# Optimization experiments

Hardware: AMD Instinct MI355X
Metric: run time of the kernel (lower is better)

## Reference

```python
import jax, jax.numpy as jnp
import numpy as np

N_ATOM, N_TOKEN = 1024, 256
C_S, C_Z, C_ATOM, C_ATOM_PAIR = 384, 128, 128, 16
EPS = 1e-5


def _layer_norm(x, w, b):
    m = jnp.mean(x, axis=-1, keepdims=True)
    v = jnp.mean(jnp.square(x - m), axis=-1, keepdims=True)
    return (x - m) * jax.lax.rsqrt(v + EPS) * w + b


def setup_inputs() -> dict:
    key = jax.random.key(0)
    ks = jax.random.split(key, 12)
    # one-hot atom -> token map (each atom belongs to exactly one token)
    tok_idx = jnp.sort(jax.random.randint(ks[0], (N_ATOM,), 0, N_TOKEN))
    a2t = jax.nn.one_hot(tok_idx, N_TOKEN, dtype=jnp.float32)  # [n_atom, n_token]
    return {
        "atom_to_token_index": a2t,
        "cl": jax.random.normal(ks[1], (N_ATOM, C_ATOM), jnp.float32),
        "plm": jax.random.normal(ks[2], (N_ATOM, N_ATOM, C_ATOM_PAIR), jnp.float32),
        "ql": jax.random.normal(ks[3], (N_ATOM, C_ATOM), jnp.float32),
        "s_trunk": jax.random.normal(ks[4], (N_TOKEN, C_S), jnp.float32),
        "zij": jax.random.normal(ks[5], (N_TOKEN, N_TOKEN, C_Z), jnp.float32),
        "rl": jax.random.normal(ks[6], (N_ATOM, 3), jnp.float32),
        "ln_s_w": jnp.ones((C_S,), jnp.float32),
        "ln_s_b": jnp.zeros((C_S,), jnp.float32),
        "W_s": jax.random.normal(ks[7], (C_S, C_ATOM), jnp.float32) / np.sqrt(C_S),
        "ln_z_w": jnp.ones((C_Z,), jnp.float32),
        "ln_z_b": jnp.zeros((C_Z,), jnp.float32),
        "W_z": jax.random.normal(ks[8], (C_Z, C_ATOM_PAIR), jnp.float32) / np.sqrt(C_Z),
        "W_r": jax.random.normal(ks[9], (3, C_ATOM), jnp.float32) / np.sqrt(3.0),
    }


def reference(atom_to_token_index, cl, plm, ql, s_trunk, zij, rl,
              ln_s_w, ln_s_b, W_s, ln_z_w, ln_z_b, W_z, W_r):
    a2t = atom_to_token_index  # one-hot [n_atom, n_token]
    # cl += Linear_s(LN_s(sum_t s_trunk[t] * a2t[a,t]))  (token->atom broadcast)
    s_atom = jnp.einsum('tc,at->ac', s_trunk, a2t)  # [n_atom, c_s]
    cl = cl + _layer_norm(s_atom, ln_s_w, ln_s_b) @ W_s
    # plm += Linear_z(LN_z(sum_{t,m} zij[t,m] * a2t[a,t] * a2t[b,m]))
    z_at = jnp.einsum('tmc,at->amc', zij, a2t)      # [n_atom, n_token, c_z]
    z_ab = jnp.einsum('amc,bm->abc', z_at, a2t)     # [n_atom, n_atom, c_z]
    plm = plm + _layer_norm(z_ab, ln_z_w, ln_z_b) @ W_z
    # ql += Linear_r(rl)
    ql = ql + rl @ W_r
    return (cl, plm, ql)
```

## Files before the change

### kernel.cpp

```cpp
#include <hip/hip_runtime.h>
#include <hip/hip_bf16.h>

#define NA 1024
#define NT 256
#define CS 384
#define CZ 128
#define CA 128
#define CP 16

typedef __attribute__((ext_vector_type(8))) short short8;
typedef __attribute__((ext_vector_type(4))) float f32x4;

__device__ __forceinline__ float bfu(unsigned short v){ return __uint_as_float(((unsigned)v) << 16); }
__device__ __forceinline__ unsigned short f2bf(float f){
  unsigned u = __float_as_uint(f);
  return (unsigned short)((u + 0x7fffu + ((u >> 16) & 1u)) >> 16);
}
__device__ __forceinline__ unsigned pack2(float lo, float hi){
  return (unsigned)f2bf(lo) | ((unsigned)f2bf(hi) << 16);
}

__device__ __forceinline__ int lbound(const unsigned short* tokL, int key){
  int lo = 0, hi = NA;
  while (lo < hi) { int mid = (lo + hi) >> 1; if ((int)tokL[mid] < key) lo = mid + 1; else hi = mid; }
  return lo;
}

__global__ __launch_bounds__(256) void prep_kernel(
    const float* __restrict__ a2t,
    const float* __restrict__ s_trunk,
    const float* __restrict__ lnsw,
    const float* __restrict__ lnsb,
    const float* __restrict__ Ws,
    unsigned short* __restrict__ tok16,
    unsigned short* __restrict__ ytok)
{
  __shared__ float redS[4], redQ[4];
  __shared__ float lnbuf[CS];
  __shared__ float part[CA];

  const int blk  = blockIdx.x;
  const int tid  = threadIdx.x;
  const int lane = tid & 63;
  const int wv   = tid >> 6;

  if (blk < 256) {
    int a = blk * 4 + wv;
    float4 u = ((const float4*)(a2t + (size_t)a * NT))[lane];
    bool hit = (u.x != 0.f) | (u.y != 0.f) | (u.z != 0.f) | (u.w != 0.f);
    unsigned long long m = __ballot(hit);
    int fl = __ffsll(m) - 1;
    if (lane == fl) {
      int t = lane * 4;
      if (u.x != 0.f)      {  }
      else if (u.y != 0.f) t += 1;
      else if (u.z != 0.f) t += 2;
      else                 t += 3;
      tok16[a] = (unsigned short)t;
    }
  } else {
    int tk = blk - 256;
    float f0 = 0.f, f1 = 0.f;
    if (tid < 192) {
      float2 v = ((const float2*)(s_trunk + (size_t)tk * CS))[tid];
      f0 = v.x; f1 = v.y;
    }
    float s = f0 + f1;
    float q = f0 * f0 + f1 * f1;
    #pragma unroll
    for (int m = 1; m < 64; m <<= 1) { s += __shfl_xor(s, m); q += __shfl_xor(q, m); }
    if (lane == 0) { redS[wv] = s; redQ[wv] = q; }
    __syncthreads();
    if (tid == 0) {
      float S = redS[0] + redS[1] + redS[2] + redS[3];
      float Q = redQ[0] + redQ[1] + redQ[2] + redQ[3];
      float mean = S * (1.f / 384.f);
      float var  = Q * (1.f / 384.f) - mean * mean;
      redS[0] = mean;
      redQ[0] = rsqrtf(var + 1e-5f);
    }
    __syncthreads();
    float mean = redS[0], rstd = redQ[0];
    if (tid < 192) {
      float2 w2 = ((const float2*)lnsw)[tid];
      float2 b2 = ((const float2*)lnsb)[tid];
      lnbuf[2 * tid]     = fmaf((f0 - mean) * rstd, w2.x, b2.x);
      lnbuf[2 * tid + 1] = fmaf((f1 - mean) * rstd, w2.y, b2.y);
    }
    __syncthreads();
    int j = tid & 127, half = tid >> 7;
    float acc = 0.f;
    int c0 = half * 192;
    #pragma unroll 8
    for (int c = c0; c < c0 + 192; ++c)
      acc = fmaf(lnbuf[c], Ws[(size_t)c * CA + j], acc);
    if (half) part[j] = acc;
    __syncthreads();
    if (!half) ytok[(size_t)tk * CA + j] = f2bf(acc + part[j]);
  }
}

__global__ __launch_bounds__(256) void main_kernel(
    const float* __restrict__ cl,
    const float* __restrict__ plm,
    const float* __restrict__ ql,
    const float* __restrict__ rl,
    const float* __restrict__ Wr,
    const float* __restrict__ zij,
    const float* __restrict__ lnzw,
    const float* __restrict__ lnzb,
    const float* __restrict__ Wz,
    const unsigned short* __restrict__ tok16,
    const unsigned short* __restrict__ ytok,
    float* __restrict__ out)
{
  const int blk = blockIdx.x;
  const int tid = threadIdx.x;

  if (blk < 1024) {
    __shared__ unsigned short tokL[NA];
    __shared__ unsigned short stage[4 * 16 * 136];
    __shared__ float wlds[64 * 16];

    const int lane = tid & 63;
    const int wv   = tid >> 6;
    const int t    = blk >> 2;
    const int m0   = (blk & 3) << 6;

    ((uint2*)tokL)[tid] = ((const uint2*)tok16)[tid];
    __syncthreads();

    int s = lbound(tokL, t);
    int e = lbound(tokL, t + 1);
    if (s == e) return;
    int S = lbound(tokL, m0);
    int E = lbound(tokL, m0 + 64);
    if (S == E) return;

    {
      int r = lane >> 2, q = lane & 3;
      int mrow = m0 + wv * 16 + r;
      const float4* zp = (const float4*)(zij + ((size_t)t * NT + mrow) * CZ + q * 32);
      float x[32];
      float sm = 0.f, ss = 0.f;
      #pragma unroll
      for (int i = 0; i < 8; ++i) {
        float4 v = zp[i];
        x[4 * i]     = v.x; x[4 * i + 1] = v.y;
        x[4 * i + 2] = v.z; x[4 * i + 3] = v.w;
        sm += (v.x + v.y) + (v.z + v.w);
        ss = fmaf(v.x, v.x, ss); ss = fmaf(v.y, v.y, ss);
        ss = fmaf(v.z, v.z, ss); ss = fmaf(v.w, v.w, ss);
      }
      sm += __shfl_xor(sm, 1); sm += __shfl_xor(sm, 2);
      ss += __shfl_xor(ss, 1); ss += __shfl_xor(ss, 2);
      float mean = sm * (1.f / 128.f);
      float var  = ss * (1.f / 128.f) - mean * mean;
      float rstd = rsqrtf(var + 1e-5f);
      unsigned short* st = stage + wv * 2176 + r * 136 + q * 32;
      const float4* lwp = (const float4*)(lnzw + q * 32);
      const float4* lbp = (const float4*)(lnzb + q * 32);
      #pragma unroll
      for (int i = 0; i < 4; ++i) {
        float4 lw0 = lwp[2 * i], lw1 = lwp[2 * i + 1];
        float4 lb0 = lbp[2 * i], lb1 = lbp[2 * i + 1];
        int c = i * 8;
        unsigned o0 = pack2(fmaf((x[c]     - mean) * rstd, lw0.x, lb0.x),
                            fmaf((x[c + 1] - mean) * rstd, lw0.y, lb0.y));
        unsigned o1 = pack2(fmaf((x[c + 2] - mean) * rstd, lw0.z, lb0.z),
                            fmaf((x[c + 3] - mean) * rstd, lw0.w, lb0.w));
        unsigned o2 = pack2(fmaf((x[c + 4] - mean) * rstd, lw1.x, lb1.x),
                            fmaf((x[c + 5] - mean) * rstd, lw1.y, lb1.y));
        unsigned o3 = pack2(fmaf((x[c + 6] - mean) * rstd, lw1.z, lb1.z),
                            fmaf((x[c + 7] - mean) * rstd, lw1.w, lb1.w));
        uint4 ov; ov.x = o0; ov.y = o1; ov.z = o2; ov.w = o3;
        ((uint4*)st)[i] = ov;
      }
      __syncthreads();
      int h = lane >> 4, lm = lane & 15;
      short8 bfrag[4];
      #pragma unroll
      for (int kk = 0; kk < 4; ++kk)
        #pragma unroll
        for (int jj = 0; jj < 8; ++jj)
          bfrag[kk][jj] = (short)f2bf(Wz[(size_t)(kk * 32 + h * 8 + jj) * CP + lm]);
      const unsigned short* sb = stage + wv * 2176;
      f32x4 acc = {0.f, 0.f, 0.f, 0.f};
      #pragma unroll
      for (int kk = 0; kk < 4; ++kk) {
        short8 af = *(const short8*)(sb + lm * 136 + kk * 32 + h * 8);
        acc = __builtin_amdgcn_mfma_f32_16x16x32_bf16(af, bfrag[kk], acc, 0, 0, 0);
      }
      #pragma unroll
      for (int jj = 0; jj < 4; ++jj)
        wlds[(wv * 16 + h * 4 + jj) * 16 + lm] = acc[jj];
    }
    __syncthreads();

    const float4* plm4 = (const float4*)plm;
    float4* out4 = (float4*)(out + (size_t)NA * CA);
    int ntask = (E - S) * 4;
    for (int a = s; a < e; ++a) {
      size_t rowbase = ((size_t)a << 10);
      for (int task = tid; task < ntask; task += 256) {
        int b = S + (task >> 2), quar = task & 3;
        int m = ((int)tokL[b] - m0) & 63;
        const float* w = wlds + m * 16 + quar * 4;
        size_t p4 = (rowbase + b) * 4 + quar;
        float4 pv = plm4[p4];
        float4 ov;
        ov.x = pv.x + w[0]; ov.y = pv.y + w[1];
        ov.z = pv.z + w[2]; ov.w = pv.w + w[3];
        out4[p4] = ov;
      }
    }
  } else if (blk < 1536) {
    int idx = (blk - 1024) * 256 + tid;
    int a = idx >> 7, j = idx & 127;
    int ta = (int)tok16[a] & 255;
    out[idx] = cl[idx] + bfu(ytok[(size_t)ta * CA + j]);
  } else {
    int idx = (blk - 1536) * 256 + tid;
    int a = idx >> 7, j = idx & 127;
    float r0 = rl[a * 3 + 0], r1 = rl[a * 3 + 1], r2 = rl[a * 3 + 2];
    float v = ql[idx];
    v = fmaf(r0, Wr[j], v);
    v = fmaf(r1, Wr[CA + j], v);
    v = fmaf(r2, Wr[2 * CA + j], v);
    out[(size_t)NA * CA + (size_t)NA * NA * CP + idx] = v;
  }
}

extern "C" void kernel_launch(void* const* d_in, const int* in_sizes, int n_in,
                              void* d_out, int out_size, void* d_ws, size_t ws_size,
                              hipStream_t stream) {
  const float* a2t     = (const float*)d_in[0];
  const float* cl      = (const float*)d_in[1];
  const float* plm     = (const float*)d_in[2];
  const float* ql      = (const float*)d_in[3];
  const float* s_trunk = (const float*)d_in[4];
  const float* zij     = (const float*)d_in[5];
  const float* rl      = (const float*)d_in[6];
  const float* lnsw    = (const float*)d_in[7];
  const float* lnsb    = (const float*)d_in[8];
  const float* Ws      = (const float*)d_in[9];
  const float* lnzw    = (const float*)d_in[10];
  const float* lnzb    = (const float*)d_in[11];
  const float* Wz      = (const float*)d_in[12];
  const float* Wr      = (const float*)d_in[13];
  float* out = (float*)d_out;

  unsigned short* tok16 = (unsigned short*)d_ws;
  unsigned short* ytok  = (unsigned short*)d_ws + NA;

  prep_kernel<<<512, 256, 0, stream>>>(a2t, s_trunk, lnsw, lnsb, Ws, tok16, ytok);
  main_kernel<<<2048, 256, 0, stream>>>(cl, plm, ql, rl, Wr, zij, lnzw, lnzb, Wz,
                                        tok16, ytok, out);
}
```

Before: 220.7 us.

## Split atom rows across two blocks per tile and batch plm loads

Each (token, m-chunk) tile now runs as two blocks, each handling alternating atom rows, which doubles the grid of pair blocks to spread the memory-bound plm streaming across more workgroups. The staging buffer and the weight table share one LDS allocation to cut shared-memory use, which needs an extra barrier. The inner loop issues four plm loads before any stores to raise memory-level parallelism. The cost is that each block recomputes the LayerNorm and MFMA projection for its tile, doubling that work.

After: 213.5 us. 3.3% less time.

```diff
diff --git a/kernel.cpp b/kernel.cpp
--- a/kernel.cpp
+++ b/kernel.cpp
@@ -117,22 +117,24 @@
   const int blk = blockIdx.x;
   const int tid = threadIdx.x;
 
-  if (blk < 1024) {
+  if (blk < 2048) {
     __shared__ unsigned short tokL[NA];
-    __shared__ unsigned short stage[4 * 16 * 136];
-    __shared__ float wlds[64 * 16];
+    __shared__ __align__(16) unsigned short ubuf[4 * 16 * 136];
+    unsigned short* stage = ubuf;
+    float* wlds = (float*)ubuf;
 
     const int lane = tid & 63;
     const int wv   = tid >> 6;
-    const int t    = blk >> 2;
-    const int m0   = (blk & 3) << 6;
+    const int t    = blk >> 3;
+    const int m0   = ((blk >> 1) & 3) << 6;
+    const int slot = blk & 1;
 
     ((uint2*)tokL)[tid] = ((const uint2*)tok16)[tid];
     __syncthreads();
 
     int s = lbound(tokL, t);
     int e = lbound(tokL, t + 1);
-    if (s == e) return;
+    if (s + slot >= e) return;
     int S = lbound(tokL, m0);
     int E = lbound(tokL, m0 + 64);
     if (S == E) return;
@@ -185,12 +187,15 @@
         for (int jj = 0; jj < 8; ++jj)
           bfrag[kk][jj] = (short)f2bf(Wz[(size_t)(kk * 32 + h * 8 + jj) * CP + lm]);
       const unsigned short* sb = stage + wv * 2176;
+      short8 af[4];
+      #pragma unroll
+      for (int kk = 0; kk < 4; ++kk)
+        af[kk] = *(const short8*)(sb + lm * 136 + kk * 32 + h * 8);
       f32x4 acc = {0.f, 0.f, 0.f, 0.f};
       #pragma unroll
-      for (int kk = 0; kk < 4; ++kk) {
-        short8 af = *(const short8*)(sb + lm * 136 + kk * 32 + h * 8);
-        acc = __builtin_amdgcn_mfma_f32_16x16x32_bf16(af, bfrag[kk], acc, 0, 0, 0);
-      }
+      for (int kk = 0; kk < 4; ++kk)
+        acc = __builtin_amdgcn_mfma_f32_16x16x32_bf16(af[kk], bfrag[kk], acc, 0, 0, 0);
+      __syncthreads();
       #pragma unroll
       for (int jj = 0; jj < 4; ++jj)
         wlds[(wv * 16 + h * 4 + jj) * 16 + lm] = acc[jj];
@@ -199,28 +204,42 @@
 
     const float4* plm4 = (const float4*)plm;
     float4* out4 = (float4*)(out + (size_t)NA * CA);
-    int ntask = (E - S) * 4;
-    for (int a = s; a < e; ++a) {
+    const int ntask = (E - S) * 4;
+    for (int a = s + slot; a < e; a += 2) {
       size_t rowbase = ((size_t)a << 10);
-      for (int task = tid; task < ntask; task += 256) {
-        int b = S + (task >> 2), quar = task & 3;
-        int m = ((int)tokL[b] - m0) & 63;
-        const float* w = wlds + m * 16 + quar * 4;
-        size_t p4 = (rowbase + b) * 4 + quar;
-        float4 pv = plm4[p4];
-        float4 ov;
-        ov.x = pv.x + w[0]; ov.y = pv.y + w[1];
-        ov.z = pv.z + w[2]; ov.w = pv.w + w[3];
-        out4[p4] = ov;
+      for (int base = 0; base < ntask; base += 1024) {
+        float4 pv[4], wv4[4];
+        size_t idx4[4];
+        bool act[4];
+        #pragma unroll
+        for (int j = 0; j < 4; ++j) {
+          int task = base + j * 256 + tid;
+          act[j] = (task < ntask);
+          int tt = act[j] ? task : 0;
+          int b = S + (tt >> 2), quar = tt & 3;
+          int m = ((int)tokL[b] - m0) & 63;
+          idx4[j] = (rowbase + b) * 4 + quar;
+          wv4[j] = *(const float4*)(wlds + m * 16 + quar * 4);
+          pv[j]  = plm4[idx4[j]];
+        }
+        #pragma unroll
+        for (int j = 0; j < 4; ++j) {
+          if (act[j]) {
+            float4 ov;
+            ov.x = pv[j].x + wv4[j].x; ov.y = pv[j].y + wv4[j].y;
+            ov.z = pv[j].z + wv4[j].z; ov.w = pv[j].w + wv4[j].w;
+            out4[idx4[j]] = ov;
+          }
+        }
       }
     }
-  } else if (blk < 1536) {
-    int idx = (blk - 1024) * 256 + tid;
+  } else if (blk < 2560) {
+    int idx = (blk - 2048) * 256 + tid;
     int a = idx >> 7, j = idx & 127;
     int ta = (int)tok16[a] & 255;
     out[idx] = cl[idx] + bfu(ytok[(size_t)ta * CA + j]);
   } else {
-    int idx = (blk - 1536) * 256 + tid;
+    int idx = (blk - 2560) * 256 + tid;
     int a = idx >> 7, j = idx & 127;
     float r0 = rl[a * 3 + 0], r1 = rl[a * 3 + 1], r2 = rl[a * 3 + 2];
     float v = ql[idx];
@@ -254,6 +273,6 @@
   unsigned short* ytok  = (unsigned short*)d_ws + NA;
 
   prep_kernel<<<512, 256, 0, stream>>>(a2t, s_trunk, lnsw, lnsb, Ws, tok16, ytok);
-  main_kernel<<<2048, 256, 0, stream>>>(cl, plm, ql, rl, Wr, zij, lnzw, lnzb, Wz,
+  main_kernel<<<3072, 256, 0, stream>>>(cl, plm, ql, rl, Wr, zij, lnzw, lnzb, Wz,
                                         tok16, ytok, out);
 }
```
